# Kernel optimization log

Hardware: AMD Instinct MI355X
Metric: run time of the kernel (lower is better)

The kernel has to match this reference:

```python
import jax, jax.numpy as jnp
import numpy as np

EMBED_DIM = 2048
NUM_EXPERTS = 64
TOP_K = 2
BATCH = 16384


def setup_inputs() -> dict:
    key = jax.random.key(0)
    kx, kw, kb = jax.random.split(key, 3)
    x = jax.random.normal(kx, (BATCH, EMBED_DIM), dtype=jnp.float32)
    # nn.Linear(embed_dim, num_experts): weight [num_experts, embed_dim], bias [num_experts]
    bound = 1.0 / np.sqrt(EMBED_DIM)
    W = jax.random.uniform(kw, (NUM_EXPERTS, EMBED_DIM), minval=-bound, maxval=bound, dtype=jnp.float32)
    b = jax.random.uniform(kb, (NUM_EXPERTS,), minval=-bound, maxval=bound, dtype=jnp.float32)
    return {"x": x, "W": W, "b": b}


def reference(x, W, b):
    # logits: (batch, num_experts)
    logits = jnp.einsum('bd,ed->be', x, W) + b
    topk_logits, topk_indices = jax.lax.top_k(logits, TOP_K)
    gates = jax.nn.softmax(topk_logits, axis=-1)
    return gates, topk_indices
```

## Files before the change

### kernel.cpp

```cpp
#include <hip/hip_runtime.h>
#include <math.h>

#define EMBED   2048
#define NEXP    64
#define BATCHN  16384
#define RT      16
#define NT_A    256
#define LCAP    16380
#define MARGIN_THRESH 4e-4f

typedef float  f32x4  __attribute__((ext_vector_type(4)));
typedef __bf16 bf16x8 __attribute__((ext_vector_type(8)));

__device__ __forceinline__ void cvt8(const float4& a, const float4& b,
                                     bf16x8& h, bf16x8& l) {
    float f[8] = {a.x, a.y, a.z, a.w, b.x, b.y, b.z, b.w};
    #pragma unroll
    for (int j = 0; j < 8; ++j) {
        __bf16 hh = (__bf16)f[j];
        h[j] = hh;
        l[j] = (__bf16)(f[j] - (float)hh);
    }
}

__global__ __launch_bounds__(256)
void pack_w_kernel(const float* __restrict__ W, __bf16* __restrict__ Wh,
                   __bf16* __restrict__ Wl, int* __restrict__ flagcnt)
{
    const int g = blockIdx.x * 256 + threadIdx.x;
    if (g == 0) *flagcnt = 0;
    const int tile = g >> 12, rem = g & 4095;
    const int kc = rem >> 6, ln = rem & 63;
    const int e = tile * 16 + (ln & 15);
    const int k = kc * 32 + (ln >> 4) * 8;
    const float* wp = W + (size_t)e * EMBED + k;
    float4 a = *(const float4*)wp, b = *(const float4*)(wp + 4);
    bf16x8 h, l;
    cvt8(a, b, h, l);
    *(bf16x8*)(Wh + (size_t)g * 8) = h;
    *(bf16x8*)(Wl + (size_t)g * 8) = l;
}

__global__ __launch_bounds__(NT_A, 4)
void gemm_topk_kernel(const float* __restrict__ x, const __bf16* __restrict__ Wh,
                      const __bf16* __restrict__ Wl, const float* __restrict__ bias,
                      float* __restrict__ out, int* __restrict__ flagcnt,
                      int* __restrict__ flaglist)
{
    __shared__ __align__(16) __bf16 Ah[2][2048];
    __shared__ __align__(16) __bf16 Al[2][2048];
    __shared__ float lg[RT][64];

    const int tid  = threadIdx.x;
    const int lane = tid & 63;
    const int w    = tid >> 6;
    const int row0 = blockIdx.x * RT;

    const float* xr = x + (size_t)(row0 + (lane & 15)) * EMBED + w * 32 + (lane >> 4) * 8;
    const __bf16* whp = Wh + ((size_t)w * 64 * 64 + lane) * 8;
    const __bf16* wlp = Wl + ((size_t)w * 64 * 64 + lane) * 8;

    f32x4 acc = {0.f, 0.f, 0.f, 0.f};

    {
        float4 a = *(const float4*)xr, b = *(const float4*)(xr + 4);
        bf16x8 h, l;
        cvt8(a, b, h, l);
        *(bf16x8*)&Ah[0][tid * 8] = h;
        *(bf16x8*)&Al[0][tid * 8] = l;
    }
    __syncthreads();

    #pragma unroll 1
    for (int s = 0; s < 16; ++s) {
        const int cur = s & 1;
        float4 qa, qb;
        if (s < 15) {
            qa = *(const float4*)(xr + (s + 1) * 128);
            qb = *(const float4*)(xr + (s + 1) * 128 + 4);
        }
        #pragma unroll
        for (int kc = 0; kc < 4; ++kc) {
            bf16x8 ah = *(bf16x8*)&Ah[cur][(kc * 64 + lane) * 8];
            bf16x8 al = *(bf16x8*)&Al[cur][(kc * 64 + lane) * 8];
            bf16x8 bh = *(const bf16x8*)(whp + (size_t)(s * 4 + kc) * 512);
            bf16x8 bl = *(const bf16x8*)(wlp + (size_t)(s * 4 + kc) * 512);
            acc = __builtin_amdgcn_mfma_f32_16x16x32_bf16(ah, bh, acc, 0, 0, 0);
            acc = __builtin_amdgcn_mfma_f32_16x16x32_bf16(ah, bl, acc, 0, 0, 0);
            acc = __builtin_amdgcn_mfma_f32_16x16x32_bf16(al, bh, acc, 0, 0, 0);
        }
        if (s < 15) {
            bf16x8 h, l;
            cvt8(qa, qb, h, l);
            *(bf16x8*)&Ah[cur ^ 1][tid * 8] = h;
            *(bf16x8*)&Al[cur ^ 1][tid * 8] = l;
        }
        __syncthreads();
    }

    const float bb = bias[w * 16 + (lane & 15)];
    #pragma unroll
    for (int q = 0; q < 4; ++q)
        lg[(lane >> 4) * 4 + q][w * 16 + (lane & 15)] = acc[q] + bb;
    __syncthreads();

    #pragma unroll 1
    for (int r = 0; r < 4; ++r) {
        const int row_l = w * 4 + r;
        float v1 = lg[row_l][lane], v2 = -INFINITY, v3 = -INFINITY;
        int   i1 = lane, i2 = 0;
        #pragma unroll
        for (int m = 1; m <= 32; m <<= 1) {
            const float o1  = __shfl_xor(v1, m, 64);
            const int   oi1 = __shfl_xor(i1, m, 64);
            const float o2  = __shfl_xor(v2, m, 64);
            const int   oi2 = __shfl_xor(i2, m, 64);
            const float o3  = __shfl_xor(v3, m, 64);
            if (o1 > v1) {
                float nv2; int ni2; float nv3;
                if (v1 > o2) { nv2 = v1; ni2 = i1;  nv3 = fmaxf(v2, o2); }
                else         { nv2 = o2; ni2 = oi2; nv3 = fmaxf(v1, o3); }
                v1 = o1; i1 = oi1; v2 = nv2; i2 = ni2; v3 = nv3;
            } else {
                if (o1 > v2) { v3 = fmaxf(v2, o2); v2 = o1; i2 = oi1; }
                else         { v3 = fmaxf(v3, o1); }
            }
        }
        if (lane == 0) {
            const int row = row0 + row_l;
            const float margin = fminf(v1 - v2, v2 - v3);
            if (margin < MARGIN_THRESH) {
                const int idx = atomicAdd(flagcnt, 1);
                if (idx < LCAP) flaglist[idx] = row;
            }
            const float e2  = __expf(v2 - v1);
            const float inv = 1.0f / (1.0f + e2);
            *(float2*)&out[row * 2]              = make_float2(inv, e2 * inv);
            *(float2*)&out[2 * BATCHN + row * 2] = make_float2((float)i1, (float)i2);
        }
    }
}

__global__ __launch_bounds__(256, 2)
void recheck_kernel(const float* __restrict__ x, const float* __restrict__ W,
                    const float* __restrict__ bias, float* __restrict__ out,
                    const int* __restrict__ flagcnt, const int* __restrict__ flaglist)
{
    __shared__ double sh[NEXP];
    const int tid = threadIdx.x;
    const int e = tid >> 2, q = tid & 3;
    int cnt = *flagcnt;
    if (cnt > LCAP) cnt = LCAP;

    #pragma unroll 1
    for (int i = blockIdx.x; i < cnt; i += gridDim.x) {
        const int row = flaglist[i];
        const float* xr = x + (size_t)row * EMBED + q * 512;
        const float* wr = W + (size_t)e * EMBED + q * 512;
        double s = 0.0;
        #pragma unroll 4
        for (int k = 0; k < 512; k += 4) {
            const float4 xv = *(const float4*)(xr + k);
            const float4 wv = *(const float4*)(wr + k);
            s += (double)xv.x * (double)wv.x;
            s += (double)xv.y * (double)wv.y;
            s += (double)xv.z * (double)wv.z;
            s += (double)xv.w * (double)wv.w;
        }
        s += __shfl_xor(s, 1, 64);
        s += __shfl_xor(s, 2, 64);
        if (q == 0) sh[e] = s + (double)bias[e];
        __syncthreads();
        if (tid == 0) {
            double v1 = -1e300, v2 = -1e300; int i1 = 0, i2 = 0;
            for (int ee = 0; ee < NEXP; ++ee) {
                const double v = sh[ee];
                if (v > v1)      { v2 = v1; i2 = i1; v1 = v; i1 = ee; }
                else if (v > v2) { v2 = v; i2 = ee; }
            }
            const double ex  = exp(v2 - v1);
            const double inv = 1.0 / (1.0 + ex);
            out[row * 2]                  = (float)inv;
            out[row * 2 + 1]              = (float)(ex * inv);
            out[2 * BATCHN + row * 2]     = (float)i1;
            out[2 * BATCHN + row * 2 + 1] = (float)i2;
        }
        __syncthreads();
    }
}

extern "C" void kernel_launch(void* const* d_in, const int* in_sizes, int n_in,
                              void* d_out, int out_size, void* d_ws, size_t ws_size,
                              hipStream_t stream) {
    const float* x = (const float*)d_in[0];
    const float* W = (const float*)d_in[1];
    const float* b = (const float*)d_in[2];
    float* out = (float*)d_out;
    int*    flagcnt  = (int*)d_ws;
    int*    flaglist = flagcnt + 4;
    __bf16* Wh = (__bf16*)((char*)d_ws + 65536);
    __bf16* Wl = (__bf16*)((char*)d_ws + 65536 + 262144);
    pack_w_kernel   <<<dim3(64),          dim3(256),  0, stream>>>(W, Wh, Wl, flagcnt);
    gemm_topk_kernel<<<dim3(BATCHN / RT), dim3(NT_A), 0, stream>>>(x, Wh, Wl, b, out, flagcnt, flaglist);
    recheck_kernel  <<<dim3(128),         dim3(256),  0, stream>>>(x, W, b, out, flagcnt, flaglist);
}
```

Baseline: 244.7 us.

## Process 32 rows per block to reuse packed weight fragments across two tiles

Each block now computes two 16-row tiles, so every loaded Wh/Wl fragment feeds two sets of MFMAs instead of one. Global weight traffic per row is halved and the grid shrinks to 512 blocks. The cost is doubled LDS and register use, with launch bounds lowered to 2 blocks per CU, so fewer waves are available to hide the x loads.

Result: no change. 240.4 us (-1.7%).

```diff
diff --git a/kernel.cpp b/kernel.cpp
--- a/kernel.cpp
+++ b/kernel.cpp
@@ -4,7 +4,7 @@
 #define EMBED   2048
 #define NEXP    64
 #define BATCHN  16384
-#define RT      16
+#define RT      32
 #define NT_A    256
 #define LCAP    16380
 #define MARGIN_THRESH 4e-4f
@@ -41,14 +41,14 @@
     *(bf16x8*)(Wl + (size_t)g * 8) = l;
 }
 
-__global__ __launch_bounds__(NT_A, 4)
+__global__ __launch_bounds__(NT_A, 2)
 void gemm_topk_kernel(const float* __restrict__ x, const __bf16* __restrict__ Wh,
                       const __bf16* __restrict__ Wl, const float* __restrict__ bias,
                       float* __restrict__ out, int* __restrict__ flagcnt,
                       int* __restrict__ flaglist)
 {
-    __shared__ __align__(16) __bf16 Ah[2][2048];
-    __shared__ __align__(16) __bf16 Al[2][2048];
+    __shared__ __align__(16) __bf16 Ah[2][4096];
+    __shared__ __align__(16) __bf16 Al[2][4096];
     __shared__ float lg[RT][64];
 
     const int tid  = threadIdx.x;
@@ -56,57 +56,74 @@
     const int w    = tid >> 6;
     const int row0 = blockIdx.x * RT;
 
-    const float* xr = x + (size_t)(row0 + (lane & 15)) * EMBED + w * 32 + (lane >> 4) * 8;
+    const float* xr0 = x + (size_t)(row0 + (lane & 15)) * EMBED + w * 32 + (lane >> 4) * 8;
+    const float* xr1 = xr0 + (size_t)16 * EMBED;
     const __bf16* whp = Wh + ((size_t)w * 64 * 64 + lane) * 8;
     const __bf16* wlp = Wl + ((size_t)w * 64 * 64 + lane) * 8;
 
-    f32x4 acc = {0.f, 0.f, 0.f, 0.f};
+    f32x4 acc0 = {0.f, 0.f, 0.f, 0.f};
+    f32x4 acc1 = {0.f, 0.f, 0.f, 0.f};
 
     {
-        float4 a = *(const float4*)xr, b = *(const float4*)(xr + 4);
         bf16x8 h, l;
-        cvt8(a, b, h, l);
+        cvt8(*(const float4*)xr0, *(const float4*)(xr0 + 4), h, l);
         *(bf16x8*)&Ah[0][tid * 8] = h;
         *(bf16x8*)&Al[0][tid * 8] = l;
+        cvt8(*(const float4*)xr1, *(const float4*)(xr1 + 4), h, l);
+        *(bf16x8*)&Ah[0][2048 + tid * 8] = h;
+        *(bf16x8*)&Al[0][2048 + tid * 8] = l;
     }
     __syncthreads();
 
     #pragma unroll 1
     for (int s = 0; s < 16; ++s) {
         const int cur = s & 1;
-        float4 qa, qb;
+        float4 qa0, qb0, qa1, qb1;
         if (s < 15) {
-            qa = *(const float4*)(xr + (s + 1) * 128);
-            qb = *(const float4*)(xr + (s + 1) * 128 + 4);
+            qa0 = *(const float4*)(xr0 + (s + 1) * 128);
+            qb0 = *(const float4*)(xr0 + (s + 1) * 128 + 4);
+            qa1 = *(const float4*)(xr1 + (s + 1) * 128);
+            qb1 = *(const float4*)(xr1 + (s + 1) * 128 + 4);
         }
         #pragma unroll
         for (int kc = 0; kc < 4; ++kc) {
-            bf16x8 ah = *(bf16x8*)&Ah[cur][(kc * 64 + lane) * 8];
-            bf16x8 al = *(bf16x8*)&Al[cur][(kc * 64 + lane) * 8];
-            bf16x8 bh = *(const bf16x8*)(whp + (size_t)(s * 4 + kc) * 512);
-            bf16x8 bl = *(const bf16x8*)(wlp + (size_t)(s * 4 + kc) * 512);
-            acc = __builtin_amdgcn_mfma_f32_16x16x32_bf16(ah, bh, acc, 0, 0, 0);
-            acc = __builtin_amdgcn_mfma_f32_16x16x32_bf16(ah, bl, acc, 0, 0, 0);
-            acc = __builtin_amdgcn_mfma_f32_16x16x32_bf16(al, bh, acc, 0, 0, 0);
+            const int ao = (kc * 64 + lane) * 8;
+            bf16x8 ah0 = *(bf16x8*)&Ah[cur][ao];
+            bf16x8 al0 = *(bf16x8*)&Al[cur][ao];
+            bf16x8 ah1 = *(bf16x8*)&Ah[cur][2048 + ao];
+            bf16x8 al1 = *(bf16x8*)&Al[cur][2048 + ao];
+            bf16x8 bh  = *(const bf16x8*)(whp + (size_t)(s * 4 + kc) * 512);
+            bf16x8 bl  = *(const bf16x8*)(wlp + (size_t)(s * 4 + kc) * 512);
+            acc0 = __builtin_amdgcn_mfma_f32_16x16x32_bf16(ah0, bh, acc0, 0, 0, 0);
+            acc0 = __builtin_amdgcn_mfma_f32_16x16x32_bf16(ah0, bl, acc0, 0, 0, 0);
+            acc0 = __builtin_amdgcn_mfma_f32_16x16x32_bf16(al0, bh, acc0, 0, 0, 0);
+            acc1 = __builtin_amdgcn_mfma_f32_16x16x32_bf16(ah1, bh, acc1, 0, 0, 0);
+            acc1 = __builtin_amdgcn_mfma_f32_16x16x32_bf16(ah1, bl, acc1, 0, 0, 0);
+            acc1 = __builtin_amdgcn_mfma_f32_16x16x32_bf16(al1, bh, acc1, 0, 0, 0);
         }
         if (s < 15) {
             bf16x8 h, l;
-            cvt8(qa, qb, h, l);
+            cvt8(qa0, qb0, h, l);
             *(bf16x8*)&Ah[cur ^ 1][tid * 8] = h;
             *(bf16x8*)&Al[cur ^ 1][tid * 8] = l;
+            cvt8(qa1, qb1, h, l);
+            *(bf16x8*)&Ah[cur ^ 1][2048 + tid * 8] = h;
+            *(bf16x8*)&Al[cur ^ 1][2048 + tid * 8] = l;
         }
         __syncthreads();
     }
 
     const float bb = bias[w * 16 + (lane & 15)];
     #pragma unroll
-    for (int q = 0; q < 4; ++q)
-        lg[(lane >> 4) * 4 + q][w * 16 + (lane & 15)] = acc[q] + bb;
+    for (int q = 0; q < 4; ++q) {
+        lg[(lane >> 4) * 4 + q][w * 16 + (lane & 15)]      = acc0[q] + bb;
+        lg[16 + (lane >> 4) * 4 + q][w * 16 + (lane & 15)] = acc1[q] + bb;
+    }
     __syncthreads();
 
     #pragma unroll 1
-    for (int r = 0; r < 4; ++r) {
-        const int row_l = w * 4 + r;
+    for (int r = 0; r < 8; ++r) {
+        const int row_l = w * 8 + r;
         float v1 = lg[row_l][lane], v2 = -INFINITY, v3 = -INFINITY;
         int   i1 = lane, i2 = 0;
         #pragma unroll
```

## Split-K across waves with 32-row tiles and register-resident x operands

Applied to the files above, without the earlier changes.

Each block now handles 32 rows instead of 16. Each of its four waves covers a quarter of the K dimension for all 64 experts, and the per-wave partial sums are reduced through shared memory at the end. Each wave converts x to bf16 hi/lo in registers directly, replacing the shared-memory staging and the per-step barriers of the old K loop. Each W fragment loaded is reused across two 16-row halves, which halves W traffic per row. The cost is more accumulator registers (occupancy hint lowered to 2), a serial reduction done by one wave, and half as many blocks.

After: 255.7 us. +4.5%, slower.

```diff
diff --git a/kernel.cpp b/kernel.cpp
--- a/kernel.cpp
+++ b/kernel.cpp
@@ -4,7 +4,7 @@
 #define EMBED   2048
 #define NEXP    64
 #define BATCHN  16384
-#define RT      16
+#define RT      32
 #define NT_A    256
 #define LCAP    16380
 #define MARGIN_THRESH 4e-4f
@@ -41,72 +41,91 @@
     *(bf16x8*)(Wl + (size_t)g * 8) = l;
 }
 
-__global__ __launch_bounds__(NT_A, 4)
+__global__ __launch_bounds__(NT_A, 2)
 void gemm_topk_kernel(const float* __restrict__ x, const __bf16* __restrict__ Wh,
                       const __bf16* __restrict__ Wl, const float* __restrict__ bias,
                       float* __restrict__ out, int* __restrict__ flagcnt,
                       int* __restrict__ flaglist)
 {
-    __shared__ __align__(16) __bf16 Ah[2][2048];
-    __shared__ __align__(16) __bf16 Al[2][2048];
+    __shared__ float shred[3][64][33];
     __shared__ float lg[RT][64];
 
     const int tid  = threadIdx.x;
     const int lane = tid & 63;
-    const int w    = tid >> 6;
+    const int ks   = tid >> 6;
     const int row0 = blockIdx.x * RT;
 
-    const float* xr = x + (size_t)(row0 + (lane & 15)) * EMBED + w * 32 + (lane >> 4) * 8;
-    const __bf16* whp = Wh + ((size_t)w * 64 * 64 + lane) * 8;
-    const __bf16* wlp = Wl + ((size_t)w * 64 * 64 + lane) * 8;
-
-    f32x4 acc = {0.f, 0.f, 0.f, 0.f};
-
-    {
-        float4 a = *(const float4*)xr, b = *(const float4*)(xr + 4);
-        bf16x8 h, l;
-        cvt8(a, b, h, l);
-        *(bf16x8*)&Ah[0][tid * 8] = h;
-        *(bf16x8*)&Al[0][tid * 8] = l;
+    const float* xr0 = x + (size_t)(row0 + (lane & 15)) * EMBED + ks * 512 + ((lane >> 4) & 3) * 8;
+    const float* xr1 = xr0 + (size_t)16 * EMBED;
+    const __bf16* whb = Wh + ((size_t)(ks * 16) * 64 + lane) * 8;
+    const __bf16* wlb = Wl + ((size_t)(ks * 16) * 64 + lane) * 8;
+
+    f32x4 acc[2][4] = {};
+
+    float4 a0 = *(const float4*)(xr0), b0 = *(const float4*)(xr0 + 4);
+    float4 a1 = *(const float4*)(xr1), b1 = *(const float4*)(xr1 + 4);
+
+    #pragma unroll 1
+    for (int kc = 0; kc < 16; ++kc) {
+        float4 na0, nb0, na1, nb1;
+        if (kc < 15) {
+            na0 = *(const float4*)(xr0 + (kc + 1) * 32);
+            nb0 = *(const float4*)(xr0 + (kc + 1) * 32 + 4);
+            na1 = *(const float4*)(xr1 + (kc + 1) * 32);
+            nb1 = *(const float4*)(xr1 + (kc + 1) * 32 + 4);
+        }
+        bf16x8 ah0, al0, ah1, al1;
+        cvt8(a0, b0, ah0, al0);
+        cvt8(a1, b1, ah1, al1);
+        #pragma unroll
+        for (int t = 0; t < 4; ++t) {
+            bf16x8 bh = *(const bf16x8*)(whb + (size_t)t * 32768 + (size_t)kc * 512);
+            bf16x8 bl = *(const bf16x8*)(wlb + (size_t)t * 32768 + (size_t)kc * 512);
+            acc[0][t] = __builtin_amdgcn_mfma_f32_16x16x32_bf16(ah0, bh, acc[0][t], 0, 0, 0);
+            acc[0][t] = __builtin_amdgcn_mfma_f32_16x16x32_bf16(ah0, bl, acc[0][t], 0, 0, 0);
+            acc[0][t] = __builtin_amdgcn_mfma_f32_16x16x32_bf16(al0, bh, acc[0][t], 0, 0, 0);
+            acc[1][t] = __builtin_amdgcn_mfma_f32_16x16x32_bf16(ah1, bh, acc[1][t], 0, 0, 0);
+            acc[1][t] = __builtin_amdgcn_mfma_f32_16x16x32_bf16(ah1, bl, acc[1][t], 0, 0, 0);
+            acc[1][t] = __builtin_amdgcn_mfma_f32_16x16x32_bf16(al1, bh, acc[1][t], 0, 0, 0);
+        }
+        a0 = na0; b0 = nb0; a1 = na1; b1 = nb1;
+    }
+
+    if (ks > 0) {
+        #pragma unroll
+        for (int rh = 0; rh < 2; ++rh)
+            #pragma unroll
+            for (int t = 0; t < 4; ++t)
+                #pragma unroll
+                for (int q = 0; q < 4; ++q)
+                    shred[ks - 1][lane][(rh * 4 + t) * 4 + q] = acc[rh][t][q];
     }
     __syncthreads();
+    if (ks == 0) {
+        #pragma unroll
+        for (int w = 0; w < 3; ++w)
+            #pragma unroll
+            for (int rh = 0; rh < 2; ++rh)
+                #pragma unroll
+                for (int t = 0; t < 4; ++t)
+                    #pragma unroll
+                    for (int q = 0; q < 4; ++q)
+                        acc[rh][t][q] += shred[w][lane][(rh * 4 + t) * 4 + q];
+        #pragma unroll
+        for (int t = 0; t < 4; ++t) {
+            const float bb = bias[t * 16 + (lane & 15)];
+            #pragma unroll
+            for (int q = 0; q < 4; ++q) {
+                lg[((lane >> 4) & 3) * 4 + q][t * 16 + (lane & 15)]      = acc[0][t][q] + bb;
+                lg[16 + ((lane >> 4) & 3) * 4 + q][t * 16 + (lane & 15)] = acc[1][t][q] + bb;
+            }
+        }
+    }
+    __syncthreads();
 
     #pragma unroll 1
-    for (int s = 0; s < 16; ++s) {
-        const int cur = s & 1;
-        float4 qa, qb;
-        if (s < 15) {
-            qa = *(const float4*)(xr + (s + 1) * 128);
-            qb = *(const float4*)(xr + (s + 1) * 128 + 4);
-        }
-        #pragma unroll
-        for (int kc = 0; kc < 4; ++kc) {
-            bf16x8 ah = *(bf16x8*)&Ah[cur][(kc * 64 + lane) * 8];
-            bf16x8 al = *(bf16x8*)&Al[cur][(kc * 64 + lane) * 8];
-            bf16x8 bh = *(const bf16x8*)(whp + (size_t)(s * 4 + kc) * 512);
-            bf16x8 bl = *(const bf16x8*)(wlp + (size_t)(s * 4 + kc) * 512);
-            acc = __builtin_amdgcn_mfma_f32_16x16x32_bf16(ah, bh, acc, 0, 0, 0);
-            acc = __builtin_amdgcn_mfma_f32_16x16x32_bf16(ah, bl, acc, 0, 0, 0);
-            acc = __builtin_amdgcn_mfma_f32_16x16x32_bf16(al, bh, acc, 0, 0, 0);
-        }
-        if (s < 15) {
-            bf16x8 h, l;
-            cvt8(qa, qb, h, l);
-            *(bf16x8*)&Ah[cur ^ 1][tid * 8] = h;
-            *(bf16x8*)&Al[cur ^ 1][tid * 8] = l;
-        }
-        __syncthreads();
-    }
-
-    const float bb = bias[w * 16 + (lane & 15)];
-    #pragma unroll
-    for (int q = 0; q < 4; ++q)
-        lg[(lane >> 4) * 4 + q][w * 16 + (lane & 15)] = acc[q] + bb;
-    __syncthreads();
-
-    #pragma unroll 1
-    for (int r = 0; r < 4; ++r) {
-        const int row_l = w * 4 + r;
+    for (int r = 0; r < 8; ++r) {
+        const int row_l = ks * 8 + r;
         float v1 = lg[row_l][lane], v2 = -INFINITY, v3 = -INFINITY;
         int   i1 = lane, i2 = 0;
         #pragma unroll
```
